# Kernel optimization log

Measured on AMD Instinct MI355X. Metric: run time of the kernel, lower is better.

## Reference

```python
import jax, jax.numpy as jnp
import numpy as np

M = 128      # molecules
L = 256      # max nodes per molecule (padding length)
H = 768      # hidden_size
NH = 12      # num_heads
HD = H // NH # head_dim
N = M * L    # total flat nodes
EPS = 1e-5


def setup_inputs() -> dict:
    key = jax.random.key(0)
    ks = jax.random.split(key, 12)
    s = 1.0 / np.sqrt(H)
    atom_features = jax.random.normal(ks[0], (N, H), dtype=jnp.float32)
    a_starts = jnp.arange(M, dtype=jnp.int32) * L
    a_sizes = jax.random.randint(ks[1], (M,), L // 2, L + 1, dtype=jnp.int32)
    inp = {
        'atom_features': atom_features,
        'Wq': jax.random.normal(ks[2], (H, H), jnp.float32) * s,
        'bq': jnp.zeros((H,), jnp.float32),
        'Wk': jax.random.normal(ks[3], (H, H), jnp.float32) * s,
        'bk': jnp.zeros((H,), jnp.float32),
        'Wv': jax.random.normal(ks[4], (H, H), jnp.float32) * s,
        'bv': jnp.zeros((H,), jnp.float32),
        'Wo': jax.random.normal(ks[5], (H, H), jnp.float32) * s,
        'bo': jnp.zeros((H,), jnp.float32),
        'gamma': jnp.ones((H,), jnp.float32),
        'beta': jnp.zeros((H,), jnp.float32),
        'a_starts': a_starts,
        'a_sizes': a_sizes,
    }
    return inp


def reference(atom_features, Wq, bq, Wk, bk, Wv, bv, Wo, bo, gamma, beta,
              a_starts, a_sizes):
    scale = HD ** -0.5
    pos = jnp.arange(L, dtype=jnp.int32)
    idx = a_starts[:, None] + pos[None, :]                      # [M, L]
    mask = pos[None, :] < a_sizes[:, None]                      # [M, L] valid nodes
    x = atom_features[idx] * mask[..., None]                    # [M, L, H]

    def proj(W, b):
        y = jnp.einsum('mlh,oh->mlo', x, W) + b                 # torch Linear: x @ W.T + b
        return y.reshape(M, L, NH, HD).transpose(0, 2, 1, 3)    # [M, NH, L, HD]

    q, k, v = proj(Wq, bq), proj(Wk, bk), proj(Wv, bv)
    scores = jnp.einsum('mhqd,mhkd->mhqk', q, k) * scale        # [M, NH, L, L]
    scores = jnp.where(mask[:, None, None, :], scores, -1e9)
    attn = jax.nn.softmax(scores, axis=-1)
    ctx = jnp.einsum('mhqk,mhkd->mhqd', attn, v)                # [M, NH, L, HD]
    ctx = ctx.transpose(0, 2, 1, 3).reshape(M, L, H)
    out = jnp.einsum('mlh,oh->mlo', ctx, Wo) + bo

    y = out + x                                                 # residual
    mu = jnp.mean(y, axis=-1, keepdims=True)
    var = jnp.mean((y - mu) ** 2, axis=-1, keepdims=True)
    y = (y - mu) * jax.lax.rsqrt(var + EPS) * gamma + beta
    y = y * mask[..., None]

    enhanced = jnp.zeros_like(atom_features).at[idx.reshape(-1)].set(
        y.reshape(-1, H))
    return enhanced
```

## Files before the change

kernel.cpp:

```cpp
#include <hip/hip_runtime.h>
#include <hip/hip_bf16.h>
#include <stdint.h>

#define M_MOL 128
#define L_SEQ 256
#define H_DIM 768
#define NH_   12
#define HD_   64
#define N_TOT (M_MOL * L_SEQ)

typedef __attribute__((ext_vector_type(8))) short bf16x8;
typedef __attribute__((ext_vector_type(4))) float f32x4;
typedef __attribute__((ext_vector_type(8))) unsigned short u16x8;
typedef __hip_bfloat16 bf16;

__device__ __forceinline__ float bf2f(bf16 x){ return __bfloat162float(x); }
__device__ __forceinline__ bf16 f2bf(float x){ return __float2bfloat16(x); }
__device__ __forceinline__ float bfbits2f(unsigned short u){
    return __uint_as_float(((unsigned)u) << 16);
}
__device__ __forceinline__ unsigned pk2(float lo, float hi){
    bf16 a = f2bf(lo), b = f2bf(hi);
    unsigned short ua, ub;
    __builtin_memcpy(&ua, &a, 2);
    __builtin_memcpy(&ub, &b, 2);
    return (unsigned)ua | ((unsigned)ub << 16);
}

typedef const __attribute__((address_space(1))) unsigned int* as1_u32p;
typedef __attribute__((address_space(3))) unsigned int* as3_u32p;
__device__ __forceinline__ void async_ld16(const void* g, const void* l) {
    __builtin_amdgcn_global_load_lds((as1_u32p)(unsigned long long)g,
                                     (as3_u32p)(unsigned int)(unsigned long long)l,
                                     16, 0, 0);
}

__global__ __launch_bounds__(256)
void cvt_all(const float* __restrict__ af, const float* __restrict__ Wq,
             const float* __restrict__ Wk, const float* __restrict__ Wv,
             const float* __restrict__ Wo,
             bf16* __restrict__ afb, bf16* __restrict__ Wcat, bf16* __restrict__ Wobf)
{
    const int b = blockIdx.x;
    const float* src; bf16* dst; int local;
    if (b < 12288) { src = af; dst = afb; local = b; }
    else {
        int r = b - 12288;
        int mat = r / 288; local = r % 288;
        src = mat==0 ? Wq : mat==1 ? Wk : mat==2 ? Wv : Wo;
        dst = (mat < 3) ? (Wcat + (size_t)mat*589824) : Wobf;
    }
    const size_t off = ((size_t)local*256 + threadIdx.x)*8;
    float4 a = *(const float4*)(src + off);
    float4 c = *(const float4*)(src + off + 4);
    uint4 o = { pk2(a.x,a.y), pk2(a.z,a.w), pk2(c.x,c.y), pk2(c.z,c.w) };
    *(uint4*)(dst + off) = o;
}

__global__ __launch_bounds__(256, 2)
void gemm_qkv(const bf16* __restrict__ A, const bf16* __restrict__ W,
              const float* __restrict__ bq, const float* __restrict__ bk,
              const float* __restrict__ bv,
              bf16* __restrict__ qb, bf16* __restrict__ kb, bf16* __restrict__ vb)
{
    __shared__ __align__(16) bf16 As[128*32];
    __shared__ __align__(16) bf16 Bs[128*32];
    const int t = threadIdx.x;
    const int colBlk  = blockIdx.x >> 8;
    const int rowBase = (blockIdx.x & 255) * 128;
    const int colBase = colBlk * 128;
    const int w = t >> 6, lane = t & 63, quad = lane >> 4, r16 = lane & 15;
    const int wr = w >> 1, wc = w & 1;
    const int ldsW = w << 6;

    f32x4 acc[4][4];
#pragma unroll
    for (int i = 0; i < 4; ++i)
#pragma unroll
        for (int j = 0; j < 4; ++j) acc[i][j] = (f32x4){0.f,0.f,0.f,0.f};

    for (int k0 = 0; k0 < 768; k0 += 32) {
        int u0 = t, u1 = t + 256;
        async_ld16(&A[(size_t)(rowBase + (u0>>2))*768 + k0 + (u0&3)*8],
                   &As[(size_t)ldsW*8]);
        async_ld16(&A[(size_t)(rowBase + (u1>>2))*768 + k0 + (u1&3)*8],
                   &As[(size_t)(256 + ldsW)*8]);
        async_ld16(&W[(size_t)(colBase + (u0>>2))*768 + k0 + (u0&3)*8],
                   &Bs[(size_t)ldsW*8]);
        async_ld16(&W[(size_t)(colBase + (u1>>2))*768 + k0 + (u1&3)*8],
                   &Bs[(size_t)(256 + ldsW)*8]);
        __syncthreads();
        bf16x8 af[4], bfr[4];
#pragma unroll
        for (int ti = 0; ti < 4; ++ti)
            af[ti] = *(const bf16x8*)(&As[(wr*64 + ti*16 + r16)*32 + quad*8]);
#pragma unroll
        for (int tj = 0; tj < 4; ++tj)
            bfr[tj] = *(const bf16x8*)(&Bs[(wc*64 + tj*16 + r16)*32 + quad*8]);
#pragma unroll
        for (int ti = 0; ti < 4; ++ti)
#pragma unroll
            for (int tj = 0; tj < 4; ++tj)
                acc[ti][tj] = __builtin_amdgcn_mfma_f32_16x16x32_bf16(
                    af[ti], bfr[tj], acc[ti][tj], 0, 0, 0);
        __syncthreads();
    }
    const int sel = colBlk / 6;
    const float* bias = sel==0 ? bq : sel==1 ? bk : bv;
    bf16* C = sel==0 ? qb : sel==1 ? kb : vb;
    const int colSec = colBase - sel*768;
#pragma unroll
    for (int tj = 0; tj < 4; ++tj) {
        int col = colSec + wc*64 + tj*16 + r16;
        float bb = bias[col];
#pragma unroll
        for (int ti = 0; ti < 4; ++ti) {
            int row0 = rowBase + wr*64 + ti*16 + quad*4;
#pragma unroll
            for (int rr = 0; rr < 4; ++rr)
                C[(size_t)(row0+rr)*768 + col] = f2bf(acc[ti][tj][rr] + bb);
        }
    }
}

__global__ __launch_bounds__(256, 2)
void gemm_o(const bf16* __restrict__ A, const bf16* __restrict__ W,
            const float* __restrict__ bo, bf16* __restrict__ C)
{
    __shared__ __align__(16) bf16 As[128*32];
    __shared__ __align__(16) bf16 Bs[128*32];
    const int t = threadIdx.x;
    const int colBase = (blockIdx.x >> 8) * 128;
    const int rowBase = (blockIdx.x & 255) * 128;
    const int w = t >> 6, lane = t & 63, quad = lane >> 4, r16 = lane & 15;
    const int wr = w >> 1, wc = w & 1;
    const int ldsW = w << 6;

    f32x4 acc[4][4];
#pragma unroll
    for (int i = 0; i < 4; ++i)
#pragma unroll
        for (int j = 0; j < 4; ++j) acc[i][j] = (f32x4){0.f,0.f,0.f,0.f};

    for (int k0 = 0; k0 < 768; k0 += 32) {
        int u0 = t, u1 = t + 256;
        async_ld16(&A[(size_t)(rowBase + (u0>>2))*768 + k0 + (u0&3)*8],
                   &As[(size_t)ldsW*8]);
        async_ld16(&A[(size_t)(rowBase + (u1>>2))*768 + k0 + (u1&3)*8],
                   &As[(size_t)(256 + ldsW)*8]);
        async_ld16(&W[(size_t)(colBase + (u0>>2))*768 + k0 + (u0&3)*8],
                   &Bs[(size_t)ldsW*8]);
        async_ld16(&W[(size_t)(colBase + (u1>>2))*768 + k0 + (u1&3)*8],
                   &Bs[(size_t)(256 + ldsW)*8]);
        __syncthreads();
        bf16x8 af[4], bfr[4];
#pragma unroll
        for (int ti = 0; ti < 4; ++ti)
            af[ti] = *(const bf16x8*)(&As[(wr*64 + ti*16 + r16)*32 + quad*8]);
#pragma unroll
        for (int tj = 0; tj < 4; ++tj)
            bfr[tj] = *(const bf16x8*)(&Bs[(wc*64 + tj*16 + r16)*32 + quad*8]);
#pragma unroll
        for (int ti = 0; ti < 4; ++ti)
#pragma unroll
            for (int tj = 0; tj < 4; ++tj)
                acc[ti][tj] = __builtin_amdgcn_mfma_f32_16x16x32_bf16(
                    af[ti], bfr[tj], acc[ti][tj], 0, 0, 0);
        __syncthreads();
    }
#pragma unroll
    for (int tj = 0; tj < 4; ++tj) {
        int col = colBase + wc*64 + tj*16 + r16;
        float bb = bo[col];
#pragma unroll
        for (int ti = 0; ti < 4; ++ti) {
            int row0 = rowBase + wr*64 + ti*16 + quad*4;
#pragma unroll
            for (int rr = 0; rr < 4; ++rr)
                C[(size_t)(row0+rr)*768 + col] = f2bf(acc[ti][tj][rr] + bb);
        }
    }
}

__global__ __launch_bounds__(256, 2)
void attn_kernel(const bf16* __restrict__ qbuf, const bf16* __restrict__ kbuf,
                 bf16* vctx, const int* __restrict__ a_sizes)
{
    __shared__ __align__(16) bf16 VT[64*264];
    __shared__ __align__(16) bf16 P[4*16*264];

    const int b = blockIdx.x;
    const int m = b / NH_, nh = b % NH_;
    const int t = threadIdx.x;
    const int w = t >> 6, lane = t & 63, quad = lane >> 4, r16 = lane & 15;
    const int size = a_sizes[m];
    const size_t headOff = (size_t)m*L_SEQ*768 + nh*64;

    {
        const int k0 = (t & 127) * 2;
        const int dh = (t >> 7) * 32;
        const bf16* v0 = vctx + headOff + (size_t)k0*768 + dh;
        const bf16* v1 = v0 + 768;
        u16x8 r0[4], r1[4];
#pragma unroll
        for (int c = 0; c < 4; ++c) {
            r0[c] = *(const u16x8*)(v0 + c*8);
            r1[c] = *(const u16x8*)(v1 + c*8);
        }
#pragma unroll
        for (int c = 0; c < 4; ++c)
#pragma unroll
            for (int j = 0; j < 8; ++j) {
                unsigned val = (unsigned)r0[c][j] | ((unsigned)r1[c][j] << 16);
                *(unsigned*)(&VT[(size_t)(dh + c*8 + j)*264 + k0]) = val;
            }
    }
    __syncthreads();

    bf16x8 kf0[16], kf1[16];
#pragma unroll
    for (int kt = 0; kt < 16; ++kt) {
        const bf16* krow = kbuf + headOff + (size_t)(kt*16 + r16)*768 + quad*8;
        kf0[kt] = *(const bf16x8*)(krow);
        kf1[kt] = *(const bf16x8*)(krow + 32);
    }

    bf16* Pw = P + w*16*264;
    for (int pass = 0; pass < 4; ++pass) {
        const int qrow0 = pass*64 + w*16;
        bf16x8 aq0, aq1;
        {
            const bf16* qrow = qbuf + headOff + (size_t)(qrow0 + r16)*768 + quad*8;
            aq0 = *(const bf16x8*)(qrow);
            aq1 = *(const bf16x8*)(qrow + 32);
        }
        f32x4 S[16];
#pragma unroll
        for (int kt = 0; kt < 16; ++kt) {
            f32x4 s = (f32x4){0.f,0.f,0.f,0.f};
            s = __builtin_amdgcn_mfma_f32_16x16x32_bf16(aq0, kf0[kt], s, 0, 0, 0);
            s = __builtin_amdgcn_mfma_f32_16x16x32_bf16(aq1, kf1[kt], s, 0, 0, 0);
            S[kt] = s;
        }
        float mrow[4] = {-1e30f,-1e30f,-1e30f,-1e30f};
#pragma unroll
        for (int kt = 0; kt < 16; ++kt) {
            int key = kt*16 + r16;
#pragma unroll
            for (int rr = 0; rr < 4; ++rr) {
                float s = S[kt][rr] * 0.125f;
                if (key >= size) s = -1e9f;
                S[kt][rr] = s;
                mrow[rr] = fmaxf(mrow[rr], s);
            }
        }
#pragma unroll
        for (int msk = 1; msk < 16; msk <<= 1)
#pragma unroll
            for (int rr = 0; rr < 4; ++rr)
                mrow[rr] = fmaxf(mrow[rr], __shfl_xor(mrow[rr], msk));
        float lrow[4] = {0.f,0.f,0.f,0.f};
#pragma unroll
        for (int kt = 0; kt < 16; ++kt) {
#pragma unroll
            for (int rr = 0; rr < 4; ++rr) {
                float p = __expf(S[kt][rr] - mrow[rr]);
                lrow[rr] += p;
                Pw[(quad*4+rr)*264 + kt*16 + r16] = f2bf(p);
            }
        }
#pragma unroll
        for (int msk = 1; msk < 16; msk <<= 1)
#pragma unroll
            for (int rr = 0; rr < 4; ++rr)
                lrow[rr] += __shfl_xor(lrow[rr], msk);
        asm volatile("s_waitcnt lgkmcnt(0)" ::: "memory");

        bf16x8 pa[8];
#pragma unroll
        for (int kb2 = 0; kb2 < 8; ++kb2)
            pa[kb2] = *(const bf16x8*)(&Pw[r16*264 + kb2*32 + quad*8]);
        float inv[4];
#pragma unroll
        for (int rr = 0; rr < 4; ++rr) inv[rr] = 1.f / lrow[rr];
#pragma unroll
        for (int dt = 0; dt < 4; ++dt) {
            f32x4 c = (f32x4){0.f,0.f,0.f,0.f};
#pragma unroll
            for (int kb2 = 0; kb2 < 8; ++kb2) {
                bf16x8 vb8 = *(const bf16x8*)(&VT[(dt*16 + r16)*264 + kb2*32 + quad*8]);
                c = __builtin_amdgcn_mfma_f32_16x16x32_bf16(pa[kb2], vb8, c, 0, 0, 0);
            }
#pragma unroll
            for (int rr = 0; rr < 4; ++rr) {
                int q = qrow0 + quad*4 + rr;
                vctx[headOff + (size_t)q*768 + dt*16 + r16] = f2bf(c[rr] * inv[rr]);
            }
        }
    }
}

__global__ __launch_bounds__(256, 4)
void ln_kernel(const bf16* __restrict__ proj, const float* __restrict__ af,
               const float* __restrict__ gamma, const float* __restrict__ beta,
               const int* __restrict__ a_sizes, float* __restrict__ out)
{
    const int w = threadIdx.x >> 6, lane = threadIdx.x & 63;
    const int n = blockIdx.x * 4 + w;
    const int m = n >> 8, l = n & 255;
    const int size = a_sizes[m];
    float* orow = out + (size_t)n * 768;
    if (l >= size) {
        float4 z = {0.f,0.f,0.f,0.f};
#pragma unroll
        for (int i = 0; i < 3; ++i) *(float4*)(&orow[i*256 + lane*4]) = z;
        return;
    }
    const bf16*  prow = proj + (size_t)n * 768;
    const float* xrow = af   + (size_t)n * 768;
    float y[3][4];
    float s = 0.f;
#pragma unroll
    for (int i = 0; i < 3; ++i) {
        int c = i*256 + lane*4;
        float4 xv = *(const float4*)(&xrow[c]);
        ushort4 pv = *(const ushort4*)(&prow[c]);
        y[i][0] = xv.x + bfbits2f(pv.x);
        y[i][1] = xv.y + bfbits2f(pv.y);
        y[i][2] = xv.z + bfbits2f(pv.z);
        y[i][3] = xv.w + bfbits2f(pv.w);
        s += y[i][0] + y[i][1] + y[i][2] + y[i][3];
    }
#pragma unroll
    for (int msk = 1; msk < 64; msk <<= 1) s += __shfl_xor(s, msk);
    float mu = s * (1.f/768.f);
    float v = 0.f;
#pragma unroll
    for (int i = 0; i < 3; ++i)
#pragma unroll
        for (int j = 0; j < 4; ++j) { float d = y[i][j] - mu; v += d*d; }
#pragma unroll
    for (int msk = 1; msk < 64; msk <<= 1) v += __shfl_xor(v, msk);
    float rstd = rsqrtf(v * (1.f/768.f) + 1e-5f);
#pragma unroll
    for (int i = 0; i < 3; ++i) {
        int c = i*256 + lane*4;
        float4 gv = *(const float4*)(&gamma[c]);
        float4 bv = *(const float4*)(&beta[c]);
        float4 o;
        o.x = (y[i][0] - mu) * rstd * gv.x + bv.x;
        o.y = (y[i][1] - mu) * rstd * gv.y + bv.y;
        o.z = (y[i][2] - mu) * rstd * gv.z + bv.z;
        o.w = (y[i][3] - mu) * rstd * gv.w + bv.w;
        *(float4*)(&orow[c]) = o;
    }
}

extern "C" void kernel_launch(void* const* d_in, const int* in_sizes, int n_in,
                              void* d_out, int out_size, void* d_ws, size_t ws_size,
                              hipStream_t stream)
{
    (void)in_sizes; (void)n_in; (void)out_size; (void)ws_size;
    const float* af    = (const float*)d_in[0];
    const float* Wq    = (const float*)d_in[1];
    const float* bq    = (const float*)d_in[2];
    const float* Wk    = (const float*)d_in[3];
    const float* bk    = (const float*)d_in[4];
    const float* Wv    = (const float*)d_in[5];
    const float* bv    = (const float*)d_in[6];
    const float* Wo    = (const float*)d_in[7];
    const float* bo    = (const float*)d_in[8];
    const float* gamma = (const float*)d_in[9];
    const float* beta  = (const float*)d_in[10];
    const int* a_sizes = (const int*)d_in[12];
    float* outp = (float*)d_out;

    bf16* qb = (bf16*)d_ws;
    bf16* kb = qb + (size_t)N_TOT * 768;
    bf16* vb = kb + (size_t)N_TOT * 768;
    bf16* afb  = (bf16*)d_out;
    bf16* Wcat = afb + (size_t)N_TOT * 768;
    bf16* Wobf = Wcat + (size_t)2304 * 768;

    cvt_all<<<dim3(12288 + 4*288), 256, 0, stream>>>(af, Wq, Wk, Wv, Wo, afb, Wcat, Wobf);
    gemm_qkv<<<dim3(18*256), 256, 0, stream>>>(afb, Wcat, bq, bk, bv, qb, kb, vb);
    attn_kernel<<<dim3(M_MOL * NH_), 256, 0, stream>>>(qb, kb, vb, a_sizes);
    gemm_o<<<dim3(6*256), 256, 0, stream>>>(vb, Wobf, bo, qb);
    ln_kernel<<<dim3(N_TOT / 4), 256, 0, stream>>>(qb, af, gamma, beta, a_sizes, outp);
}
```

Measured before the change: 521.4 us.

## Rewrite QKV and output GEMMs with 256x256 tiles and double-buffered async LDS pipeline

Both projection GEMMs now share a new core that uses 256x256 output tiles with 512 threads, a K step of 64, and double-buffered LDS fed by async global-to-LDS loads issued ahead of use. LDS reads are XOR-swizzled to avoid bank conflicts, MFMA bursts are interleaved with staged loads under raised wave priority, and blocks are remapped so each XCD works on a contiguous row band for L2 reuse. This aims to raise MFMA utilisation and cut global traffic per FLOP compared with the small single-buffered 128x128 K32 loop. In exchange it uses 128KB of LDS per block and many accumulator registers, which may limit occupancy, and its hand-written waitcnt and barrier ordering is fragile.

```diff
diff --git a/kernel.cpp b/kernel.cpp
--- a/kernel.cpp
+++ b/kernel.cpp
@@ -34,6 +34,8 @@
                                      (as3_u32p)(unsigned int)(unsigned long long)l,
                                      16, 0, 0);
 }
+
+#define MFMA16(a,b,c) __builtin_amdgcn_mfma_f32_16x16x32_bf16((a),(b),(c),0,0,0)
 
 __global__ __launch_bounds__(256)
 void cvt_all(const float* __restrict__ af, const float* __restrict__ Wq,
@@ -57,127 +59,193 @@
     *(uint4*)(dst + off) = o;
 }
 
-__global__ __launch_bounds__(256, 2)
+__device__ __forceinline__ void gemm256_core(
+    const bf16* __restrict__ Ap, const bf16* __restrict__ Wp,
+    int rowBase, int colBase, char* sm, f32x4 (&acc)[8][4])
+{
+    const int t = threadIdx.x;
+    const int w = t >> 6, lane = t & 63, quad = lane >> 4, r16 = lane & 15;
+    const int wr = w >> 2, wc = w & 3;
+    const int r0  = t >> 3;
+    const int kbe = (((t & 7) ^ (r0 & 7)) << 3);
+    const int aBase = (wr*128 + r16) * 128;
+    const int bBase = 32768 + (wc*64 + r16) * 128;
+    const int swz = (r16 & 7) << 4;
+    const int cs0 = (0  + quad*16) ^ swz;
+    const int cs1 = (64 + quad*16) ^ swz;
+
+#pragma unroll
+    for (int i = 0; i < 8; ++i)
+#pragma unroll
+        for (int j = 0; j < 4; ++j) acc[i][j] = (f32x4){0.f,0.f,0.f,0.f};
+
+    auto stage = [&](int isB, int T, int h) {
+        const bf16* g = isB ? Wp : Ap;
+        const int gr0 = (isB ? colBase : rowBase) + h*128 + r0;
+        const bf16* p0 = g + (size_t)gr0*768 + T*64 + kbe;
+        char* reg = sm + ((T&1)*65536 + isB*32768 + h*16384 + w*1024);
+        async_ld16(p0, reg);
+        async_ld16(p0 + (size_t)64*768, reg + 8192);
+    };
+
+    stage(0,0,0); stage(0,0,1); stage(1,0,0); stage(1,0,1);
+    stage(0,1,0); stage(0,1,1);
+    asm volatile("s_waitcnt vmcnt(4)" ::: "memory");
+    __builtin_amdgcn_s_barrier();
+
+    bf16x8 a0[4][2], a1[4][2], b0v[2][2], b1v[2][2];
+
+    for (int T = 0; T < 12; ++T) {
+        const char* Bf = sm + (T&1)*65536;
+
+#pragma unroll
+        for (int mi = 0; mi < 4; ++mi) {
+            a0[mi][0] = *(const bf16x8*)(Bf + aBase + mi*2048 + cs0);
+            a0[mi][1] = *(const bf16x8*)(Bf + aBase + mi*2048 + cs1);
+        }
+#pragma unroll
+        for (int ni = 0; ni < 2; ++ni) {
+            b0v[ni][0] = *(const bf16x8*)(Bf + bBase + ni*2048 + cs0);
+            b0v[ni][1] = *(const bf16x8*)(Bf + bBase + ni*2048 + cs1);
+        }
+        if (T+1 < 12) stage(1, T+1, 0);
+        __builtin_amdgcn_s_barrier();
+        asm volatile("s_waitcnt lgkmcnt(0)" ::: "memory");
+        __builtin_amdgcn_sched_barrier(0);
+        __builtin_amdgcn_s_setprio(1);
+#pragma unroll
+        for (int mi = 0; mi < 4; ++mi)
+#pragma unroll
+            for (int ni = 0; ni < 2; ++ni) {
+                acc[mi][ni] = MFMA16(a0[mi][0], b0v[ni][0], acc[mi][ni]);
+                acc[mi][ni] = MFMA16(a0[mi][1], b0v[ni][1], acc[mi][ni]);
+            }
+        __builtin_amdgcn_s_setprio(0);
+        __builtin_amdgcn_s_barrier();
+
+#pragma unroll
+        for (int mi = 0; mi < 4; ++mi) {
+            a1[mi][0] = *(const bf16x8*)(Bf + aBase + 8192 + mi*2048 + cs0);
+            a1[mi][1] = *(const bf16x8*)(Bf + aBase + 8192 + mi*2048 + cs1);
+        }
+        if (T+1 < 12) stage(1, T+1, 1);
+        __builtin_amdgcn_s_barrier();
+        asm volatile("s_waitcnt lgkmcnt(0)" ::: "memory");
+        __builtin_amdgcn_sched_barrier(0);
+        __builtin_amdgcn_s_setprio(1);
+#pragma unroll
+        for (int mi = 0; mi < 4; ++mi)
+#pragma unroll
+            for (int ni = 0; ni < 2; ++ni) {
+                acc[4+mi][ni] = MFMA16(a1[mi][0], b0v[ni][0], acc[4+mi][ni]);
+                acc[4+mi][ni] = MFMA16(a1[mi][1], b0v[ni][1], acc[4+mi][ni]);
+            }
+        __builtin_amdgcn_s_setprio(0);
+        __builtin_amdgcn_s_barrier();
+
+#pragma unroll
+        for (int ni = 0; ni < 2; ++ni) {
+            b1v[ni][0] = *(const bf16x8*)(Bf + bBase + 4096 + ni*2048 + cs0);
+            b1v[ni][1] = *(const bf16x8*)(Bf + bBase + 4096 + ni*2048 + cs1);
+        }
+        if (T+2 < 12) stage(0, T+2, 0);
+        __builtin_amdgcn_s_barrier();
+        asm volatile("s_waitcnt lgkmcnt(0)" ::: "memory");
+        __builtin_amdgcn_sched_barrier(0);
+        __builtin_amdgcn_s_setprio(1);
+#pragma unroll
+        for (int mi = 0; mi < 4; ++mi)
+#pragma unroll
+            for (int ni = 0; ni < 2; ++ni) {
+                acc[mi][2+ni] = MFMA16(a0[mi][0], b1v[ni][0], acc[mi][2+ni]);
+                acc[mi][2+ni] = MFMA16(a0[mi][1], b1v[ni][1], acc[mi][2+ni]);
+            }
+        __builtin_amdgcn_s_setprio(0);
+        __builtin_amdgcn_s_barrier();
+
+        if (T+2 < 12) stage(0, T+2, 1);
+        __builtin_amdgcn_s_barrier();
+        __builtin_amdgcn_s_setprio(1);
+#pragma unroll
+        for (int mi = 0; mi < 4; ++mi)
+#pragma unroll
+            for (int ni = 0; ni < 2; ++ni) {
+                acc[4+mi][2+ni] = MFMA16(a1[mi][0], b1v[ni][0], acc[4+mi][2+ni]);
+                acc[4+mi][2+ni] = MFMA16(a1[mi][1], b1v[ni][1], acc[4+mi][2+ni]);
+            }
+        __builtin_amdgcn_s_setprio(0);
+        if (T < 10)       { asm volatile("s_waitcnt vmcnt(4)" ::: "memory"); }
+        else if (T == 10) { asm volatile("s_waitcnt vmcnt(0)" ::: "memory"); }
+        __builtin_amdgcn_s_barrier();
+    }
+}
+
+__global__ __launch_bounds__(512, 2)
 void gemm_qkv(const bf16* __restrict__ A, const bf16* __restrict__ W,
               const float* __restrict__ bq, const float* __restrict__ bk,
               const float* __restrict__ bv,
               bf16* __restrict__ qb, bf16* __restrict__ kb, bf16* __restrict__ vb)
 {
-    __shared__ __align__(16) bf16 As[128*32];
-    __shared__ __align__(16) bf16 Bs[128*32];
+    __shared__ __align__(16) char sm[131072];
+    const int bid = blockIdx.x;
+    const int xcd = bid & 7, idx = bid >> 3;
+    const int rowBlk = xcd*16 + idx/9;
+    const int colBlk = idx - (idx/9)*9;
+    const int rowBase = rowBlk * 256;
+    const int colBase = colBlk * 256;
+
+    f32x4 acc[8][4];
+    gemm256_core(A, W, rowBase, colBase, sm, acc);
+
     const int t = threadIdx.x;
-    const int colBlk  = blockIdx.x >> 8;
-    const int rowBase = (blockIdx.x & 255) * 128;
-    const int colBase = colBlk * 128;
     const int w = t >> 6, lane = t & 63, quad = lane >> 4, r16 = lane & 15;
-    const int wr = w >> 1, wc = w & 1;
-    const int ldsW = w << 6;
-
-    f32x4 acc[4][4];
-#pragma unroll
-    for (int i = 0; i < 4; ++i)
-#pragma unroll
-        for (int j = 0; j < 4; ++j) acc[i][j] = (f32x4){0.f,0.f,0.f,0.f};
-
-    for (int k0 = 0; k0 < 768; k0 += 32) {
-        int u0 = t, u1 = t + 256;
-        async_ld16(&A[(size_t)(rowBase + (u0>>2))*768 + k0 + (u0&3)*8],
-                   &As[(size_t)ldsW*8]);
-        async_ld16(&A[(size_t)(rowBase + (u1>>2))*768 + k0 + (u1&3)*8],
-                   &As[(size_t)(256 + ldsW)*8]);
-        async_ld16(&W[(size_t)(colBase + (u0>>2))*768 + k0 + (u0&3)*8],
-                   &Bs[(size_t)ldsW*8]);
-        async_ld16(&W[(size_t)(colBase + (u1>>2))*768 + k0 + (u1&3)*8],
-                   &Bs[(size_t)(256 + ldsW)*8]);
-        __syncthreads();
-        bf16x8 af[4], bfr[4];
-#pragma unroll
-        for (int ti = 0; ti < 4; ++ti)
-            af[ti] = *(const bf16x8*)(&As[(wr*64 + ti*16 + r16)*32 + quad*8]);
-#pragma unroll
-        for (int tj = 0; tj < 4; ++tj)
-            bfr[tj] = *(const bf16x8*)(&Bs[(wc*64 + tj*16 + r16)*32 + quad*8]);
-#pragma unroll
-        for (int ti = 0; ti < 4; ++ti)
-#pragma unroll
-            for (int tj = 0; tj < 4; ++tj)
-                acc[ti][tj] = __builtin_amdgcn_mfma_f32_16x16x32_bf16(
-                    af[ti], bfr[tj], acc[ti][tj], 0, 0, 0);
-        __syncthreads();
-    }
-    const int sel = colBlk / 6;
+    const int wr = w >> 2, wc = w & 3;
+    const int sel = colBlk / 3;
     const float* bias = sel==0 ? bq : sel==1 ? bk : bv;
     bf16* C = sel==0 ? qb : sel==1 ? kb : vb;
     const int colSec = colBase - sel*768;
 #pragma unroll
-    for (int tj = 0; tj < 4; ++tj) {
-        int col = colSec + wc*64 + tj*16 + r16;
+    for (int nj = 0; nj < 4; ++nj) {
+        int col = colSec + wc*64 + nj*16 + r16;
         float bb = bias[col];
 #pragma unroll
-        for (int ti = 0; ti < 4; ++ti) {
-            int row0 = rowBase + wr*64 + ti*16 + quad*4;
+        for (int mi = 0; mi < 8; ++mi) {
+            int row0 = rowBase + wr*128 + mi*16 + quad*4;
 #pragma unroll
             for (int rr = 0; rr < 4; ++rr)
-                C[(size_t)(row0+rr)*768 + col] = f2bf(acc[ti][tj][rr] + bb);
-        }
-    }
-}
-
-__global__ __launch_bounds__(256, 2)
+                C[(size_t)(row0+rr)*768 + col] = f2bf(acc[mi][nj][rr] + bb);
+        }
+    }
+}
+
+__global__ __launch_bounds__(512, 2)
 void gemm_o(const bf16* __restrict__ A, const bf16* __restrict__ W,
             const float* __restrict__ bo, bf16* __restrict__ C)
 {
-    __shared__ __align__(16) bf16 As[128*32];
-    __shared__ __align__(16) bf16 Bs[128*32];
+    __shared__ __align__(16) char sm[131072];
+    const int bid = blockIdx.x;
+    const int xcd = bid & 7, idx = bid >> 3;
+    const int rowBlk = xcd*16 + idx/3;
+    const int colBlk = idx - (idx/3)*3;
+    const int rowBase = rowBlk * 256;
+    const int colBase = colBlk * 256;
+
+    f32x4 acc[8][4];
+    gemm256_core(A, W, rowBase, colBase, sm, acc);
+
     const int t = threadIdx.x;
-    const int colBase = (blockIdx.x >> 8) * 128;
-    const int rowBase = (blockIdx.x & 255) * 128;
     const int w = t >> 6, lane = t & 63, quad = lane >> 4, r16 = lane & 15;
-    const int wr = w >> 1, wc = w & 1;
-    const int ldsW = w << 6;
-
-    f32x4 acc[4][4];
-#pragma unroll
-    for (int i = 0; i < 4; ++i)
-#pragma unroll
-        for (int j = 0; j < 4; ++j) acc[i][j] = (f32x4){0.f,0.f,0.f,0.f};
-
-    for (int k0 = 0; k0 < 768; k0 += 32) {
-        int u0 = t, u1 = t + 256;
-        async_ld16(&A[(size_t)(rowBase + (u0>>2))*768 + k0 + (u0&3)*8],
-                   &As[(size_t)ldsW*8]);
-        async_ld16(&A[(size_t)(rowBase + (u1>>2))*768 + k0 + (u1&3)*8],
-                   &As[(size_t)(256 + ldsW)*8]);
-        async_ld16(&W[(size_t)(colBase + (u0>>2))*768 + k0 + (u0&3)*8],
-                   &Bs[(size_t)ldsW*8]);
-        async_ld16(&W[(size_t)(colBase + (u1>>2))*768 + k0 + (u1&3)*8],
-                   &Bs[(size_t)(256 + ldsW)*8]);
-        __syncthreads();
-        bf16x8 af[4], bfr[4];
-#pragma unroll
-        for (int ti = 0; ti < 4; ++ti)
-            af[ti] = *(const bf16x8*)(&As[(wr*64 + ti*16 + r16)*32 + quad*8]);
-#pragma unroll
-        for (int tj = 0; tj < 4; ++tj)
-            bfr[tj] = *(const bf16x8*)(&Bs[(wc*64 + tj*16 + r16)*32 + quad*8]);
-#pragma unroll
-        for (int ti = 0; ti < 4; ++ti)
-#pragma unroll
-            for (int tj = 0; tj < 4; ++tj)
-                acc[ti][tj] = __builtin_amdgcn_mfma_f32_16x16x32_bf16(
-                    af[ti], bfr[tj], acc[ti][tj], 0, 0, 0);
-        __syncthreads();
-    }
-#pragma unroll
-    for (int tj = 0; tj < 4; ++tj) {
-        int col = colBase + wc*64 + tj*16 + r16;
+    const int wr = w >> 2, wc = w & 3;
+#pragma unroll
+    for (int nj = 0; nj < 4; ++nj) {
+        int col = colBase + wc*64 + nj*16 + r16;
         float bb = bo[col];
 #pragma unroll
-        for (int ti = 0; ti < 4; ++ti) {
-            int row0 = rowBase + wr*64 + ti*16 + quad*4;
+        for (int mi = 0; mi < 8; ++mi) {
+            int row0 = rowBase + wr*128 + mi*16 + quad*4;
 #pragma unroll
             for (int rr = 0; rr < 4; ++rr)
-                C[(size_t)(row0+rr)*768 + col] = f2bf(acc[ti][tj][rr] + bb);
+                C[(size_t)(row0+rr)*768 + col] = f2bf(acc[mi][nj][rr] + bb);
         }
     }
 }
@@ -383,8 +451,8 @@
     bf16* Wobf = Wcat + (size_t)2304 * 768;
 
     cvt_all<<<dim3(12288 + 4*288), 256, 0, stream>>>(af, Wq, Wk, Wv, Wo, afb, Wcat, Wobf);
-    gemm_qkv<<<dim3(18*256), 256, 0, stream>>>(afb, Wcat, bq, bk, bv, qb, kb, vb);
+    gemm_qkv<<<dim3(1152), 512, 0, stream>>>(afb, Wcat, bq, bk, bv, qb, kb, vb);
     attn_kernel<<<dim3(M_MOL * NH_), 256, 0, stream>>>(qb, kb, vb, a_sizes);
-    gemm_o<<<dim3(6*256), 256, 0, stream>>>(vb, Wobf, bo, qb);
+    gemm_o<<<dim3(384), 512, 0, stream>>>(vb, Wobf, bo, qb);
     ln_kernel<<<dim3(N_TOT / 4), 256, 0, stream>>>(qb, af, gamma, beta, a_sizes, outp);
 }
```

After: 495.5 us. 1.05x faster.
